# Kernel tuning notes

Measured on AMD Instinct MI355X. Metric: run time of the kernel, lower is better.

## Reference

```python
import jax, jax.numpy as jnp
import numpy as np

GRID = 48
F = GRID * GRID        # number of mesh faces
C = 128                # channels
H = 8                  # attention heads
DH = C // H
B = 2                  # meshes in batch
WID = 256              # SelectionPrediction width


def _bfs_levels():
    """BFS flood-fill levels on a 4-connected GRIDxGRID face graph, anchor at center.
    Returns [n_levels, max_ring] int32, padded with F (dropped on scatter)."""
    c = GRID // 2
    ii, jj = np.meshgrid(np.arange(GRID), np.arange(GRID), indexing='ij')
    d = (np.abs(ii - c) + np.abs(jj - c)).reshape(-1)  # BFS depth == Manhattan dist
    L = int(d.max()) + 1
    Bd = int(np.bincount(d).max())
    idx = np.full((L, Bd), F, dtype=np.int32)
    for lv in range(L):
        faces = np.nonzero(d == lv)[0]
        idx[lv, :faces.size] = faces
    return jnp.asarray(idx)


def setup_inputs() -> dict:
    key = jax.random.key(0)
    ks = jax.random.split(key, 16)
    s = 1.0 / np.sqrt(C)
    sw = 1.0 / np.sqrt(WID)
    return {
        'x':  jax.random.normal(ks[0], (B, C, F), jnp.float32),
        # AnchorAttentionBlock projections (q/k/v/out)
        'Wq': jax.random.normal(ks[1], (C, C), jnp.float32) * s,
        'Wk': jax.random.normal(ks[2], (C, C), jnp.float32) * s,
        'Wv': jax.random.normal(ks[3], (C, C), jnp.float32) * s,
        'Wo': jax.random.normal(ks[4], (C, C), jnp.float32) * s,
        # SelectionPrediction (n_input=C, width=256, depth=3, sigmoid)
        'W1': jax.random.normal(ks[5], (C, WID), jnp.float32) * s,
        'b1': jnp.zeros((WID,), jnp.float32),
        'W2': jax.random.normal(ks[6], (WID, WID), jnp.float32) * sw,
        'b2': jnp.zeros((WID,), jnp.float32),
        'W3': jax.random.normal(ks[7], (WID, WID), jnp.float32) * sw,
        'b3': jnp.zeros((WID,), jnp.float32),
        'W4': jax.random.normal(ks[8], (WID, WID), jnp.float32) * sw,
        'b4': jnp.zeros((WID,), jnp.float32),
        'W5': jax.random.normal(ks[9], (WID, 1), jnp.float32) * sw,
        'b5': jnp.zeros((1,), jnp.float32),
        'levels_idx': _bfs_levels(),
    }


def reference(x, Wq, Wk, Wv, Wo, W1, b1, W2, b2, W3, b3, W4, b4, W5, b5, levels_idx):
    scale = 1.0 / jnp.sqrt(jnp.asarray(DH, x.dtype))

    def flood(feats):                       # feats: [F, C], one mesh
        def step(cur, idx):                 # idx: [Bd] boundary ring (pad = F)
            q = cur[idx]                                    # [Bd, C] (pad rows clamp-gather)
            qh = (q @ Wq).reshape(-1, H, DH)                # [Bd, H, DH]
            kh = (cur @ Wk).reshape(F, H, DH)               # global fftype: keys = all faces
            vh = (cur @ Wv).reshape(F, H, DH)
            att = jax.nn.softmax(jnp.einsum('bhd,fhd->bhf', qh, kh) * scale, axis=-1)
            o = jnp.einsum('bhf,fhd->bhd', att, vh).reshape(-1, C) @ Wo
            new = q + o                                     # mode='resid'
            return cur.at[idx].set(new, mode='drop'), None  # pad idx == F -> dropped
        out, _ = jax.lax.scan(step, feats, levels_idx)
        return out

    final = jax.vmap(flood)(x.transpose(0, 2, 1))           # [B, F, C]
    # SelectionPrediction on final_features.transpose(2,1)
    h = jax.nn.relu(final @ W1 + b1)
    h = jax.nn.relu(h @ W2 + b2)
    h = jax.nn.relu(h @ W3 + b3)
    h = jax.nn.relu(h @ W4 + b4)
    scores = jax.nn.sigmoid(h @ W5 + b5)                    # [B, F, 1] in [0, 1]
    return final.transpose(0, 2, 1), scores
```

## Files before the change

### kernel.cpp

```cpp
#include <hip/hip_runtime.h>
#include <hip/hip_bf16.h>
#include <stdint.h>

#define GRIDN 48
#define F 2304
#define C 128
#define H 8
#define DH 16
#define NB 2
#define WID 256
#define NLV 49
#define SMH (H * 18)
#define GLV 7

typedef __hip_bfloat16 bf16;

__device__ __forceinline__ float b2f(bf16 v) { return __bfloat162float(v); }

__global__ void k_permdetect(const void* __restrict__ x, int* __restrict__ flag,
                             int* __restrict__ permIdx, int* __restrict__ lvflags) {
    __shared__ int cnt[NLV], start[NLV];
    __shared__ int bad;
    int t = threadIdx.x;
    if (t == 0) bad = 0;
    if (t < NLV) cnt[t] = 0;
    for (int i = t; i < 2 * NLV; i += 256) lvflags[i] = 0;
    __syncthreads();
    {
        const bf16* xb = (const bf16*)x;
        int insane = 0;
        #pragma unroll
        for (int i = 0; i < 8; ++i) {
            float v = b2f(xb[t * 8 + i]);
            if (!(fabsf(v) < 1e10f)) insane = 1;
        }
        if (insane) atomicOr(&bad, 1);
    }
    for (int f = t; f < F; f += 256) {
        int d = abs(f / GRIDN - GRIDN / 2) + abs(f % GRIDN - GRIDN / 2);
        atomicAdd(&cnt[d], 1);
    }
    __syncthreads();
    if (t == 0) {
        int s = 0;
        for (int l = 0; l < NLV; ++l) { start[l] = s; s += cnt[l]; }
        *flag = bad;
    }
    __syncthreads();
    for (int f = t; f < F; f += 256) {
        int d = abs(f / GRIDN - GRIDN / 2) + abs(f % GRIDN - GRIDN / 2);
        permIdx[f] = atomicAdd(&start[d], 1);
    }
}

struct WSeg { const void* src; int off; int cnt; };
struct WSegs { WSeg s[14]; };

__global__ void k_convert(WSegs segs, const int* __restrict__ flag,
                          float* __restrict__ dst, int total) {
    int i = blockIdx.x * blockDim.x + threadIdx.x;
    if (i >= total) return;
    bool f32 = (*flag != 0);
    #pragma unroll 1
    for (int j = 0; j < 14; ++j) {
        int off = segs.s[j].off, cnt = segs.s[j].cnt;
        if (i >= off && i < off + cnt) {
            int k = i - off;
            dst[i] = f32 ? ((const float*)segs.s[j].src)[k]
                         : b2f(((const bf16*)segs.s[j].src)[k]);
            return;
        }
    }
}

__global__ void k_wtrans(const float* __restrict__ Wk, const float* __restrict__ Wv,
                         const float* __restrict__ Wo, float* __restrict__ wT) {
    int m = blockIdx.y;
    const float* s = m == 0 ? Wk : (m == 1 ? Wv : Wo);
    int c = blockIdx.x;
    int k = threadIdx.x;
    wT[((size_t)m * C + c) * C + k] = s[k * C + c];
}

__global__ void k_transpose_in(const void* __restrict__ x, const int* __restrict__ flag,
                               float* __restrict__ cur) {
    __shared__ float tile[32][33];
    bool f32 = (*flag != 0);
    int b = blockIdx.z;
    int f0 = blockIdx.x * 32, c0 = blockIdx.y * 32;
    int tx = threadIdx.x, ty = threadIdx.y;
    #pragma unroll
    for (int i = 0; i < 4; ++i) {
        int c = c0 + ty + i * 8;
        size_t idx = ((size_t)b * C + c) * F + f0 + tx;
        tile[ty + i * 8][tx] = f32 ? ((const float*)x)[idx] : b2f(((const bf16*)x)[idx]);
    }
    __syncthreads();
    #pragma unroll
    for (int i = 0; i < 4; ++i) {
        int f = f0 + ty + i * 8;
        cur[((size_t)b * F + f) * C + c0 + tx] = tile[tx][ty + i * 8];
    }
}

__global__ __launch_bounds__(128) void k_proj_init(
        const float* __restrict__ cur, const int* __restrict__ permIdx,
        const float* __restrict__ Wq, const float* __restrict__ Wk, const float* __restrict__ Wv,
        float* __restrict__ qh, float* __restrict__ khT, float* __restrict__ vhT) {
    __shared__ float rows[2][C];
    int r0 = blockIdx.x * 2;
    int tid = threadIdx.x;
    rows[0][tid] = cur[(size_t)r0 * C + tid];
    rows[1][tid] = cur[(size_t)(r0 + 1) * C + tid];
    __syncthreads();
    float aq0 = 0.f, aq1 = 0.f, ak0 = 0.f, ak1 = 0.f, av0 = 0.f, av1 = 0.f;
    for (int k = 0; k < C; ++k) {
        float wq = Wq[k * C + tid];
        float wk = Wk[k * C + tid];
        float wv = Wv[k * C + tid];
        float x0 = rows[0][k], x1 = rows[1][k];
        aq0 = fmaf(x0, wq, aq0); aq1 = fmaf(x1, wq, aq1);
        ak0 = fmaf(x0, wk, ak0); ak1 = fmaf(x1, wk, ak1);
        av0 = fmaf(x0, wv, av0); av1 = fmaf(x1, wv, av1);
    }
    const float scale = 0.25f;
    #pragma unroll
    for (int r = 0; r < 2; ++r) {
        int grow = r0 + r;
        int mesh = grow / F, face = grow % F;
        int p = permIdx[face];
        qh[(size_t)grow * C + tid] = (r == 0 ? aq0 : aq1) * scale;
        khT[((size_t)mesh * C + tid) * F + p] = r == 0 ? ak0 : ak1;
        vhT[((size_t)mesh * C + tid) * F + p] = r == 0 ? av0 : av1;
    }
}

struct Rings { int v[NLV + 1]; };
struct Pairs { int v[NLV + 1]; };

__global__ __launch_bounds__(256) void k_static(
        int Bd, Rings rings, Pairs pairs,
        const int* __restrict__ levels,
        const float* __restrict__ qh_all,
        const float* __restrict__ khT, const float* __restrict__ vhT,
        float* __restrict__ smS) {
    int bx = blockIdx.x;
    int mesh = bx & 1;
    int gp = bx >> 1;
    int lv = 0;
    while (gp >= pairs.v[lv + 1]) ++lv;
    int spair = gp - pairs.v[lv];
    int rs = rings.v[lv];
    int s0 = spair * 2, s1 = s0 + 1;
    int face0 = (s0 < Bd) ? levels[lv * Bd + s0] : F;
    int face1 = (s1 < Bd) ? levels[lv * Bd + s1] : F;
    bool a0 = (face0 >= 0 && face0 < F), a1 = (face1 >= 0 && face1 < F);
    if (!a0 && !a1) return;

    __shared__ float sQh[2][C];
    int tid = threadIdx.x;
    size_t row0 = ((size_t)mesh * F + face0) * C;
    size_t row1 = ((size_t)mesh * F + face1) * C;
    if (tid < C) sQh[0][tid] = a0 ? qh_all[row0 + tid] : 0.f;
    else { int c = tid - C; sQh[1][c] = a1 ? qh_all[row1 + c] : 0.f; }
    __syncthreads();

    int head = tid >> 5, sub = tid & 31;
    float q0[DH], q1[DH];
    #pragma unroll
    for (int d = 0; d < DH; ++d) { q0[d] = sQh[0][head * DH + d]; q1[d] = sQh[1][head * DH + d]; }

    const float* Kb = khT + ((size_t)mesh * C + head * DH) * F;
    const float* Vb = vhT + ((size_t)mesh * C + head * DH) * F;

    float m0 = -1e30f, l0 = 0.f, m1 = -1e30f, l1 = 0.f;
    float acc0[DH], acc1[DH];
    #pragma unroll
    for (int d = 0; d < DH; ++d) { acc0[d] = 0.f; acc1[d] = 0.f; }

    int base0 = rs & ~127;
    for (int base = base0; base < F; base += 128) {
        int p4 = base + 4 * sub;
        float sx0 = 0, sy0 = 0, sz0 = 0, sw0 = 0;
        float sx1 = 0, sy1 = 0, sz1 = 0, sw1 = 0;
        #pragma unroll
        for (int d = 0; d < DH; ++d) {
            float4 kk = *(const float4*)(Kb + d * F + p4);
            float a = q0[d], b = q1[d];
            sx0 = fmaf(a, kk.x, sx0); sy0 = fmaf(a, kk.y, sy0);
            sz0 = fmaf(a, kk.z, sz0); sw0 = fmaf(a, kk.w, sw0);
            sx1 = fmaf(b, kk.x, sx1); sy1 = fmaf(b, kk.y, sy1);
            sz1 = fmaf(b, kk.z, sz1); sw1 = fmaf(b, kk.w, sw1);
        }
        float g0 = 1.f, g1 = 1.f, g2 = 1.f, g3 = 1.f;
        if (base < rs) {
            g0 = (p4     >= rs) ? 1.f : 0.f; g1 = (p4 + 1 >= rs) ? 1.f : 0.f;
            g2 = (p4 + 2 >= rs) ? 1.f : 0.f; g3 = (p4 + 3 >= rs) ? 1.f : 0.f;
        }
        float mx0 = fmaxf(fmaxf(sx0, sy0), fmaxf(sz0, sw0));
        float mn0 = fmaxf(m0, mx0);
        float c0 = __expf(m0 - mn0);
        float px0 = __expf(sx0 - mn0) * g0, py0 = __expf(sy0 - mn0) * g1;
        float pz0 = __expf(sz0 - mn0) * g2, pw0 = __expf(sw0 - mn0) * g3;
        l0 = fmaf(l0, c0, px0 + py0 + pz0 + pw0);
        m0 = mn0;
        float mx1 = fmaxf(fmaxf(sx1, sy1), fmaxf(sz1, sw1));
        float mn1 = fmaxf(m1, mx1);
        float c1e = __expf(m1 - mn1);
        float px1 = __expf(sx1 - mn1) * g0, py1 = __expf(sy1 - mn1) * g1;
        float pz1 = __expf(sz1 - mn1) * g2, pw1 = __expf(sw1 - mn1) * g3;
        l1 = fmaf(l1, c1e, px1 + py1 + pz1 + pw1);
        m1 = mn1;
        #pragma unroll
        for (int d = 0; d < DH; ++d) {
            float4 vv = *(const float4*)(Vb + d * F + p4);
            float w0 = fmaf(px0, vv.x, fmaf(py0, vv.y, fmaf(pz0, vv.z, pw0 * vv.w)));
            float w1 = fmaf(px1, vv.x, fmaf(py1, vv.y, fmaf(pz1, vv.z, pw1 * vv.w)));
            acc0[d] = fmaf(acc0[d], c0, w0);
            acc1[d] = fmaf(acc1[d], c1e, w1);
        }
    }

    #pragma unroll
    for (int w = 16; w >= 1; w >>= 1) {
        float mo = __shfl_xor(m0, w), lo = __shfl_xor(l0, w);
        float mn = fmaxf(m0, mo);
        float ca = __expf(m0 - mn), cb = __expf(mo - mn);
        l0 = l0 * ca + lo * cb;
        #pragma unroll
        for (int d = 0; d < DH; ++d) {
            float ao = __shfl_xor(acc0[d], w);
            acc0[d] = acc0[d] * ca + ao * cb;
        }
        m0 = mn;
        mo = __shfl_xor(m1, w); lo = __shfl_xor(l1, w);
        mn = fmaxf(m1, mo);
        ca = __expf(m1 - mn); cb = __expf(mo - mn);
        l1 = l1 * ca + lo * cb;
        #pragma unroll
        for (int d = 0; d < DH; ++d) {
            float ao = __shfl_xor(acc1[d], w);
            acc1[d] = acc1[d] * ca + ao * cb;
        }
        m1 = mn;
    }
    if (sub == 0) {
        if (a0) {
            float* S = smS + (size_t)(mesh * F + face0) * SMH + head * 18;
            S[0] = m0; S[1] = l0;
            #pragma unroll
            for (int d = 0; d < DH; ++d) S[2 + d] = acc0[d];
        }
        if (a1) {
            float* S = smS + (size_t)(mesh * F + face1) * SMH + head * 18;
            S[0] = m1; S[1] = l1;
            #pragma unroll
            for (int d = 0; d < DH; ++d) S[2 + d] = acc1[d];
        }
    }
}

struct Grp { int lv0; int rs0; int bofs[GLV + 1]; int rs[GLV]; int re[GLV]; int ns[GLV]; };

__global__ __launch_bounds__(256, 3) void k_group(
        int Bd, Grp grp,
        const int* __restrict__ levels, const int* __restrict__ permIdx,
        const float* __restrict__ qh_all, float* __restrict__ cur,
        float* __restrict__ khT, float* __restrict__ vhT,
        const float* __restrict__ smS,
        const float* __restrict__ WkT, const float* __restrict__ WvT,
        const float* __restrict__ WoT,
        float* __restrict__ stgK, float* __restrict__ stgV,
        int* __restrict__ lvflags) {
    int bx = blockIdx.x;
    int g = 0;
    while (bx >= grp.bofs[g + 1]) ++g;
    int lb = bx - grp.bofs[g];
    int mesh = lb & 1;
    int spair = lb >> 1;
    int lv = grp.lv0 + g;
    int rs0 = grp.rs0;

    int s0 = spair * 2, s1 = s0 + 1;
    int face0 = (s0 < Bd) ? levels[lv * Bd + s0] : F;
    int face1 = (s1 < Bd) ? levels[lv * Bd + s1] : F;
    bool a0 = (face0 >= 0 && face0 < F), a1 = (face1 >= 0 && face1 < F);

    __shared__ __attribute__((aligned(16))) float sQh[2][C], sQ[2][C], sRed[2][C], sNew2[2][C];
    __shared__ float sL[2][H];
    int tid = threadIdx.x;
    size_t row0 = ((size_t)mesh * F + face0) * C;
    size_t row1 = ((size_t)mesh * F + face1) * C;
    if (tid < C) {
        if (a0) { sQ[0][tid] = cur[row0 + tid]; sQh[0][tid] = qh_all[row0 + tid]; }
        else    { sQ[0][tid] = 0.f; sQh[0][tid] = 0.f; }
    } else {
        int c = tid - C;
        if (a1) { sQ[1][c] = cur[row1 + c]; sQh[1][c] = qh_all[row1 + c]; }
        else    { sQ[1][c] = 0.f; sQh[1][c] = 0.f; }
    }
    __syncthreads();

    int head = tid >> 5, sub = tid & 31;
    float q0[DH], q1[DH];
    #pragma unroll
    for (int d = 0; d < DH; ++d) { q0[d] = sQh[0][head * DH + d]; q1[d] = sQh[1][head * DH + d]; }

    const float* Kb = khT + ((size_t)mesh * C + head * DH) * F;
    const float* Vb = vhT + ((size_t)mesh * C + head * DH) * F;

    float m0 = -1e30f, l0 = 0.f, m1 = -1e30f, l1 = 0.f;
    float acc0[DH], acc1[DH];
    #pragma unroll
    for (int d = 0; d < DH; ++d) { acc0[d] = 0.f; acc1[d] = 0.f; }

    for (int base = 0; base < rs0; base += 128) {
        int p4 = base + 4 * sub;
        float sx0 = 0, sy0 = 0, sz0 = 0, sw0 = 0;
        float sx1 = 0, sy1 = 0, sz1 = 0, sw1 = 0;
        #pragma unroll
        for (int d = 0; d < DH; ++d) {
            float4 kk = *(const float4*)(Kb + d * F + p4);
            float a = q0[d], b = q1[d];
            sx0 = fmaf(a, kk.x, sx0); sy0 = fmaf(a, kk.y, sy0);
            sz0 = fmaf(a, kk.z, sz0); sw0 = fmaf(a, kk.w, sw0);
            sx1 = fmaf(b, kk.x, sx1); sy1 = fmaf(b, kk.y, sy1);
            sz1 = fmaf(b, kk.z, sz1); sw1 = fmaf(b, kk.w, sw1);
        }
        float g0 = 1.f, g1 = 1.f, g2 = 1.f, g3 = 1.f;
        if (base + 128 > rs0) {
            g0 = (p4     < rs0) ? 1.f : 0.f; g1 = (p4 + 1 < rs0) ? 1.f : 0.f;
            g2 = (p4 + 2 < rs0) ? 1.f : 0.f; g3 = (p4 + 3 < rs0) ? 1.f : 0.f;
        }
        float mx0 = fmaxf(fmaxf(sx0, sy0), fmaxf(sz0, sw0));
        float mn0 = fmaxf(m0, mx0);
        float c0 = __expf(m0 - mn0);
        float px0 = __expf(sx0 - mn0) * g0, py0 = __expf(sy0 - mn0) * g1;
        float pz0 = __expf(sz0 - mn0) * g2, pw0 = __expf(sw0 - mn0) * g3;
        l0 = fmaf(l0, c0, px0 + py0 + pz0 + pw0);
        m0 = mn0;
        float mx1 = fmaxf(fmaxf(sx1, sy1), fmaxf(sz1, sw1));
        float mn1 = fmaxf(m1, mx1);
        float c1e = __expf(m1 - mn1);
        float px1 = __expf(sx1 - mn1) * g0, py1 = __expf(sy1 - mn1) * g1;
        float pz1 = __expf(sz1 - mn1) * g2, pw1 = __expf(sw1 - mn1) * g3;
        l1 = fmaf(l1, c1e, px1 + py1 + pz1 + pw1);
        m1 = mn1;
        #pragma unroll
        for (int d = 0; d < DH; ++d) {
            float4 vv = *(const float4*)(Vb + d * F + p4);
            float w0 = fmaf(px0, vv.x, fmaf(py0, vv.y, fmaf(pz0, vv.z, pw0 * vv.w)));
            float w1 = fmaf(px1, vv.x, fmaf(py1, vv.y, fmaf(pz1, vv.z, pw1 * vv.w)));
            acc0[d] = fmaf(acc0[d], c0, w0);
            acc1[d] = fmaf(acc1[d], c1e, w1);
        }
    }

    for (int gp = 0; gp < g; ++gp) {
        if (tid == 0) {
            int need = grp.ns[gp];
            int* fl = &lvflags[(grp.lv0 + gp) * 2 + mesh];
            int guard = 0;
            while (__hip_atomic_load(fl, __ATOMIC_RELAXED, __HIP_MEMORY_SCOPE_AGENT) < need
                   && guard < (1 << 22)) {
                __builtin_amdgcn_s_sleep(1);
                ++guard;
            }
        }
        __syncthreads();
        int frs = grp.rs[gp], fre = grp.re[gp];
        for (int p = frs + sub; p < fre; p += 32) {
            const unsigned long long* kc =
                (const unsigned long long*)(stgK + ((size_t)mesh * F + p) * C + head * DH);
            const unsigned long long* vc =
                (const unsigned long long*)(stgV + ((size_t)mesh * F + p) * C + head * DH);
            float s0v = 0.f, s1v = 0.f;
            #pragma unroll
            for (int d2 = 0; d2 < DH / 2; ++d2) {
                unsigned long long kw = __hip_atomic_load(kc + d2, __ATOMIC_RELAXED,
                                                          __HIP_MEMORY_SCOPE_AGENT);
                float2 kf = *(float2*)&kw;
                s0v = fmaf(q0[2 * d2], kf.x, s0v); s0v = fmaf(q0[2 * d2 + 1], kf.y, s0v);
                s1v = fmaf(q1[2 * d2], kf.x, s1v); s1v = fmaf(q1[2 * d2 + 1], kf.y, s1v);
            }
            float vv[DH];
            #pragma unroll
            for (int d2 = 0; d2 < DH / 2; ++d2) {
                unsigned long long vw = __hip_atomic_load(vc + d2, __ATOMIC_RELAXED,
                                                          __HIP_MEMORY_SCOPE_AGENT);
                float2 vf = *(float2*)&vw;
                vv[2 * d2] = vf.x; vv[2 * d2 + 1] = vf.y;
            }
            {
                float mn = fmaxf(m0, s0v);
                float c = __expf(m0 - mn), pw = __expf(s0v - mn);
                l0 = l0 * c + pw;
                #pragma unroll
                for (int d = 0; d < DH; ++d) acc0[d] = fmaf(acc0[d], c, pw * vv[d]);
                m0 = mn;
            }
            {
                float mn = fmaxf(m1, s1v);
                float c = __expf(m1 - mn), pw = __expf(s1v - mn);
                l1 = l1 * c + pw;
                #pragma unroll
                for (int d = 0; d < DH; ++d) acc1[d] = fmaf(acc1[d], c, pw * vv[d]);
                m1 = mn;
            }
        }
    }

    #pragma unroll
    for (int w = 16; w >= 1; w >>= 1) {
        float mo = __shfl_xor(m0, w), lo = __shfl_xor(l0, w);
        float mn = fmaxf(m0, mo);
        float ca = __expf(m0 - mn), cb = __expf(mo - mn);
        l0 = l0 * ca + lo * cb;
        #pragma unroll
        for (int d = 0; d < DH; ++d) {
            float ao = __shfl_xor(acc0[d], w);
            acc0[d] = acc0[d] * ca + ao * cb;
        }
        m0 = mn;
        mo = __shfl_xor(m1, w); lo = __shfl_xor(l1, w);
        mn = fmaxf(m1, mo);
        ca = __expf(m1 - mn); cb = __expf(mo - mn);
        l1 = l1 * ca + lo * cb;
        #pragma unroll
        for (int d = 0; d < DH; ++d) {
            float ao = __shfl_xor(acc1[d], w);
            acc1[d] = acc1[d] * ca + ao * cb;
        }
        m1 = mn;
    }
    if (sub == 0) {
        {
            int fr = a0 ? face0 : 0;
            const float* S = smS + (size_t)(mesh * F + fr) * SMH + head * 18;
            float ms = S[0], ls = S[1];
            float mn = fmaxf(m0, ms);
            float ca = __expf(m0 - mn), cb = __expf(ms - mn);
            sL[0][head] = l0 * ca + ls * cb;
            #pragma unroll
            for (int d = 0; d < DH; ++d)
                sRed[0][head * DH + d] = fmaf(acc0[d], ca, S[2 + d] * cb);
        }
        {
            int fr = a1 ? face1 : 0;
            const float* S = smS + (size_t)(mesh * F + fr) * SMH + head * 18;
            float ms = S[0], ls = S[1];
            float mn = fmaxf(m1, ms);
            float ca = __expf(m1 - mn), cb = __expf(ms - mn);
            sL[1][head] = l1 * ca + ls * cb;
            #pragma unroll
            for (int d = 0; d < DH; ++d)
                sRed[1][head * DH + d] = fmaf(acc1[d], ca, S[2 + d] * cb);
        }
    }
    __syncthreads();
    if (tid < C) sRed[0][tid] = sRed[0][tid] / sL[0][tid >> 4];
    else { int c = tid - C; sRed[1][c] = sRed[1][c] / sL[1][c >> 4]; }
    __syncthreads();

    bool doStage = (g != GLV - 1);
    {
        int j = tid >> 7;
        int c = tid & 127;
        bool act = j == 0 ? a0 : a1;
        float o = 0.f;
        const float4* WoR = (const float4*)(WoT + (size_t)c * C);
        const float4* Rr  = (const float4*)(&sRed[j][0]);
        #pragma unroll
        for (int k4 = 0; k4 < C / 4; ++k4) {
            float4 w = WoR[k4];
            float4 r = Rr[k4];
            o = fmaf(r.x, w.x, o); o = fmaf(r.y, w.y, o);
            o = fmaf(r.z, w.z, o); o = fmaf(r.w, w.w, o);
        }
        float nv = sQ[j][c] + o;
        sNew2[j][c] = nv;
        if (act) cur[(j == 0 ? row0 : row1) + c] = nv;
    }
    __syncthreads();
    #pragma unroll 1
    for (int j = 0; j < 2; ++j) {
        bool act = j == 0 ? a0 : a1;
        if (!act) continue;
        int facej = j == 0 ? face0 : face1;
        int p = permIdx[facej];
        int c = tid & 127;
        const float* WT = (tid < C) ? WkT : WvT;
        float a = 0.f;
        const float4* Wr = (const float4*)(WT + (size_t)c * C);
        const float4* Nr = (const float4*)(&sNew2[j][0]);
        #pragma unroll
        for (int k4 = 0; k4 < C / 4; ++k4) {
            float4 w = Wr[k4];
            float4 x = Nr[k4];
            a = fmaf(x.x, w.x, a); a = fmaf(x.y, w.y, a);
            a = fmaf(x.z, w.z, a); a = fmaf(x.w, w.w, a);
        }
        if (tid < C) {
            khT[((size_t)mesh * C + c) * F + p] = a;
            if (doStage)
                __hip_atomic_store(stgK + ((size_t)mesh * F + p) * C + c, a,
                                   __ATOMIC_RELAXED, __HIP_MEMORY_SCOPE_AGENT);
        } else {
            vhT[((size_t)mesh * C + c) * F + p] = a;
            if (doStage)
                __hip_atomic_store(stgV + ((size_t)mesh * F + p) * C + c, a,
                                   __ATOMIC_RELAXED, __HIP_MEMORY_SCOPE_AGENT);
        }
    }
    __syncthreads();
    if (doStage && tid == 0)
        __hip_atomic_fetch_add(&lvflags[lv * 2 + mesh], 1,
                               __ATOMIC_RELAXED, __HIP_MEMORY_SCOPE_AGENT);
}

__global__ __launch_bounds__(256) void k_mlp(
        const float* __restrict__ cur,
        const float* __restrict__ W1, const float* __restrict__ b1,
        const float* __restrict__ W2, const float* __restrict__ b2,
        const float* __restrict__ W3, const float* __restrict__ b3,
        const float* __restrict__ W4, const float* __restrict__ b4,
        const float* __restrict__ W5, const float* __restrict__ b5,
        float* __restrict__ out_scores) {
    __shared__ float sIn[2][C];
    __shared__ float sA[2][WID];
    __shared__ float sB[2][WID];
    int tid = threadIdx.x;
    int r0 = blockIdx.x * 2;
    for (int i = tid; i < 2 * C; i += 256) sIn[i >> 7][i & 127] = cur[(size_t)r0 * C + i];
    __syncthreads();
    {
        float a0 = 0.f, a1 = 0.f;
        for (int k = 0; k < C; ++k) {
            float w = W1[k * WID + tid];
            a0 = fmaf(sIn[0][k], w, a0);
            a1 = fmaf(sIn[1][k], w, a1);
        }
        float bias = b1[tid];
        sA[0][tid] = fmaxf(a0 + bias, 0.f);
        sA[1][tid] = fmaxf(a1 + bias, 0.f);
    }
    __syncthreads();
    {
        float a0 = 0.f, a1 = 0.f;
        for (int k = 0; k < WID; ++k) {
            float w = W2[k * WID + tid];
            a0 = fmaf(sA[0][k], w, a0);
            a1 = fmaf(sA[1][k], w, a1);
        }
        float bias = b2[tid];
        sB[0][tid] = fmaxf(a0 + bias, 0.f);
        sB[1][tid] = fmaxf(a1 + bias, 0.f);
    }
    __syncthreads();
    {
        float a0 = 0.f, a1 = 0.f;
        for (int k = 0; k < WID; ++k) {
            float w = W3[k * WID + tid];
            a0 = fmaf(sB[0][k], w, a0);
            a1 = fmaf(sB[1][k], w, a1);
        }
        float bias = b3[tid];
        sA[0][tid] = fmaxf(a0 + bias, 0.f);
        sA[1][tid] = fmaxf(a1 + bias, 0.f);
    }
    __syncthreads();
    {
        float a0 = 0.f, a1 = 0.f;
        for (int k = 0; k < WID; ++k) {
            float w = W4[k * WID + tid];
            a0 = fmaf(sA[0][k], w, a0);
            a1 = fmaf(sA[1][k], w, a1);
        }
        float bias = b4[tid];
        sB[0][tid] = fmaxf(a0 + bias, 0.f);
        sB[1][tid] = fmaxf(a1 + bias, 0.f);
    }
    __syncthreads();
    if (tid < 2) {
        float a = b5[0];
        for (int k = 0; k < WID; ++k) a = fmaf(sB[tid][k], W5[k], a);
        out_scores[r0 + tid] = 1.f / (1.f + __expf(-a));
    }
}

__global__ void k_transpose_out(const float* __restrict__ cur, float* __restrict__ out) {
    __shared__ float tile[32][33];
    int b = blockIdx.z;
    int f0 = blockIdx.x * 32, c0 = blockIdx.y * 32;
    int tx = threadIdx.x, ty = threadIdx.y;
    #pragma unroll
    for (int i = 0; i < 4; ++i) {
        int f = f0 + ty + i * 8;
        tile[ty + i * 8][tx] = cur[((size_t)b * F + f) * C + c0 + tx];
    }
    __syncthreads();
    #pragma unroll
    for (int i = 0; i < 4; ++i) {
        int c = c0 + ty + i * 8;
        out[((size_t)b * C + c) * F + f0 + tx] = tile[tx][ty + i * 8];
    }
}

extern "C" void kernel_launch(void* const* d_in, const int* in_sizes, int n_in,
                              void* d_out, int out_size, void* d_ws, size_t ws_size,
                              hipStream_t stream) {
    const int* levels = (const int*)d_in[15];
    int Bd = in_sizes[15] / NLV;

    const size_t n = (size_t)NB * F * C;
    float* cur  = (float*)d_ws;
    float* qh   = cur + n;
    float* khT  = qh + n;
    float* vhT  = khT + n;
    float* wbuf = vhT + n;
    float* wT   = wbuf + 296196;
    int*   permIdx = (int*)(wT + 49152);
    int*   flag = permIdx + F;
    int*   lvflags = flag + 1;
    float* smS  = (float*)(permIdx + 2404);
    float* stgK = smS + (size_t)NB * F * SMH;
    float* stgV = stgK + n;

    const int oWq = 0,       oWk = 16384,  oWv = 32768,  oWo = 49152;
    const int oW1 = 65536,   oB1 = 98304;
    const int oW2 = 98560,   oB2 = 164096;
    const int oW3 = 164352,  oB3 = 229888;
    const int oW4 = 230144,  oB4 = 295680;
    const int oW5 = 295936,  oB5 = 296192;
    const int wtot = 296193;

    WSegs segs = {{
        { d_in[1],  oWq, 16384 }, { d_in[2],  oWk, 16384 },
        { d_in[3],  oWv, 16384 }, { d_in[4],  oWo, 16384 },
        { d_in[5],  oW1, 32768 }, { d_in[6],  oB1, 256 },
        { d_in[7],  oW2, 65536 }, { d_in[8],  oB2, 256 },
        { d_in[9],  oW3, 65536 }, { d_in[10], oB3, 256 },
        { d_in[11], oW4, 65536 }, { d_in[12], oB4, 256 },
        { d_in[13], oW5, 256 },   { d_in[14], oB5, 1 },
    }};

    Rings rings;
    Pairs pairs;
    int totPairs = 0;
    {
        int cnt[NLV];
        for (int l = 0; l < NLV; ++l) cnt[l] = 0;
        for (int i = 0; i < GRIDN; ++i)
            for (int j = 0; j < GRIDN; ++j)
                cnt[(i < 24 ? 24 - i : i - 24) + (j < 24 ? 24 - j : j - 24)]++;
        rings.v[0] = 0;
        pairs.v[0] = 0;
        for (int l = 0; l < NLV; ++l) {
            rings.v[l + 1] = rings.v[l] + cnt[l];
            pairs.v[l + 1] = pairs.v[l] + (cnt[l] + 1) / 2;
        }
        totPairs = pairs.v[NLV];
    }

    float* out0 = (float*)d_out;
    float* out1 = out0 + (size_t)NB * C * F;

    k_permdetect<<<1, 256, 0, stream>>>(d_in[0], flag, permIdx, lvflags);
    k_convert<<<(wtot + 255) / 256, 256, 0, stream>>>(segs, flag, wbuf, wtot);
    k_wtrans<<<dim3(C, 3), C, 0, stream>>>(wbuf + oWk, wbuf + oWv, wbuf + oWo, wT);
    k_transpose_in<<<dim3(F / 32, C / 32, NB), dim3(32, 8), 0, stream>>>(d_in[0], flag, cur);
    k_proj_init<<<(NB * F) / 2, 128, 0, stream>>>(cur, permIdx, wbuf + oWq, wbuf + oWk, wbuf + oWv,
                                                  qh, khT, vhT);

    k_static<<<2 * totPairs, 256, 0, stream>>>(Bd, rings, pairs, levels, qh, khT, vhT, smS);

    for (int lv0 = 0; lv0 < NLV; lv0 += GLV) {
        Grp grp;
        grp.lv0 = lv0;
        grp.rs0 = rings.v[lv0];
        grp.bofs[0] = 0;
        for (int g = 0; g < GLV; ++g) {
            int lv = lv0 + g;
            int rs = rings.v[lv], re = rings.v[lv + 1];
            int ns = (re - rs + 1) / 2;
            grp.rs[g] = rs;
            grp.re[g] = re;
            grp.ns[g] = ns;
            grp.bofs[g + 1] = grp.bofs[g] + 2 * ns;
        }
        k_group<<<grp.bofs[GLV], 256, 0, stream>>>(Bd, grp, levels, permIdx, qh, cur,
                                                   khT, vhT, smS,
                                                   wT, wT + 16384, wT + 32768,
                                                   stgK, stgV, lvflags);
    }

    k_mlp<<<(NB * F) / 2, 256, 0, stream>>>(cur, wbuf + oW1, wbuf + oB1, wbuf + oW2, wbuf + oB2,
                                            wbuf + oW3, wbuf + oB3, wbuf + oW4, wbuf + oB4,
                                            wbuf + oW5, wbuf + oB5, out1);
    k_transpose_out<<<dim3(F / 32, C / 32, NB), dim3(32, 8), 0, stream>>>(cur, out0);
}
```

Before: 1.467 ms.

## Replace grouped level launches with single persistent flood kernel using per-level flags

Replaces the seven grouped launches, each covering seven BFS levels, with one k_flood launch over all level pairs. Blocks now wait on per-level completion flags and read a per-mesh 'levels done' counter to decide which prefix they can fold in bulk. K and V updates are written straight into the transposed khT/vhT with atomic stores, which removes the separate stgK/stgV staging buffers. The bulk pass loses its float4 vectorised loads for scalar atomic column loads, and cross-level dependencies now rely only on spin-waits inside one grid, which risks long stalls if dependent blocks are scheduled before their producers.

```diff
diff --git a/kernel.cpp b/kernel.cpp
--- a/kernel.cpp
+++ b/kernel.cpp
@@ -11,7 +11,6 @@
 #define WID 256
 #define NLV 49
 #define SMH (H * 18)
-#define GLV 7
 
 typedef __hip_bfloat16 bf16;
 
@@ -24,7 +23,7 @@
     int t = threadIdx.x;
     if (t == 0) bad = 0;
     if (t < NLV) cnt[t] = 0;
-    for (int i = t; i < 2 * NLV; i += 256) lvflags[i] = 0;
+    for (int i = t; i < 2 * NLV + 2; i += 256) lvflags[i] = 0;
     __syncthreads();
     {
         const bf16* xb = (const bf16*)x;
@@ -260,26 +259,21 @@
     }
 }
 
-struct Grp { int lv0; int rs0; int bofs[GLV + 1]; int rs[GLV]; int re[GLV]; int ns[GLV]; };
-
-__global__ __launch_bounds__(256, 3) void k_group(
-        int Bd, Grp grp,
+__global__ __launch_bounds__(256, 4) void k_flood(
+        int Bd, Rings rings, Pairs pairs,
         const int* __restrict__ levels, const int* __restrict__ permIdx,
         const float* __restrict__ qh_all, float* __restrict__ cur,
         float* __restrict__ khT, float* __restrict__ vhT,
         const float* __restrict__ smS,
         const float* __restrict__ WkT, const float* __restrict__ WvT,
         const float* __restrict__ WoT,
-        float* __restrict__ stgK, float* __restrict__ stgV,
-        int* __restrict__ lvflags) {
+        int* __restrict__ lvflags, int* __restrict__ lvdone) {
     int bx = blockIdx.x;
-    int g = 0;
-    while (bx >= grp.bofs[g + 1]) ++g;
-    int lb = bx - grp.bofs[g];
-    int mesh = lb & 1;
-    int spair = lb >> 1;
-    int lv = grp.lv0 + g;
-    int rs0 = grp.rs0;
+    int mesh = bx & 1;
+    int gp2 = bx >> 1;
+    int lv = 0;
+    while (gp2 >= pairs.v[lv + 1]) ++lv;
+    int spair = gp2 - pairs.v[lv];
 
     int s0 = spair * 2, s1 = s0 + 1;
     int face0 = (s0 < Bd) ? levels[lv * Bd + s0] : F;
@@ -306,109 +300,63 @@
     #pragma unroll
     for (int d = 0; d < DH; ++d) { q0[d] = sQh[0][head * DH + d]; q1[d] = sQh[1][head * DH + d]; }
 
-    const float* Kb = khT + ((size_t)mesh * C + head * DH) * F;
-    const float* Vb = vhT + ((size_t)mesh * C + head * DH) * F;
+    float* Kb = khT + ((size_t)mesh * C + head * DH) * F;
+    float* Vb = vhT + ((size_t)mesh * C + head * DH) * F;
 
     float m0 = -1e30f, l0 = 0.f, m1 = -1e30f, l1 = 0.f;
     float acc0[DH], acc1[DH];
     #pragma unroll
     for (int d = 0; d < DH; ++d) { acc0[d] = 0.f; acc1[d] = 0.f; }
 
-    for (int base = 0; base < rs0; base += 128) {
-        int p4 = base + 4 * sub;
-        float sx0 = 0, sy0 = 0, sz0 = 0, sw0 = 0;
-        float sx1 = 0, sy1 = 0, sz1 = 0, sw1 = 0;
-        #pragma unroll
-        for (int d = 0; d < DH; ++d) {
-            float4 kk = *(const float4*)(Kb + d * F + p4);
-            float a = q0[d], b = q1[d];
-            sx0 = fmaf(a, kk.x, sx0); sy0 = fmaf(a, kk.y, sy0);
-            sz0 = fmaf(a, kk.z, sz0); sw0 = fmaf(a, kk.w, sw0);
-            sx1 = fmaf(b, kk.x, sx1); sy1 = fmaf(b, kk.y, sy1);
-            sz1 = fmaf(b, kk.z, sz1); sw1 = fmaf(b, kk.w, sw1);
-        }
-        float g0 = 1.f, g1 = 1.f, g2 = 1.f, g3 = 1.f;
-        if (base + 128 > rs0) {
-            g0 = (p4     < rs0) ? 1.f : 0.f; g1 = (p4 + 1 < rs0) ? 1.f : 0.f;
-            g2 = (p4 + 2 < rs0) ? 1.f : 0.f; g3 = (p4 + 3 < rs0) ? 1.f : 0.f;
-        }
-        float mx0 = fmaxf(fmaxf(sx0, sy0), fmaxf(sz0, sw0));
-        float mn0 = fmaxf(m0, mx0);
-        float c0 = __expf(m0 - mn0);
-        float px0 = __expf(sx0 - mn0) * g0, py0 = __expf(sy0 - mn0) * g1;
-        float pz0 = __expf(sz0 - mn0) * g2, pw0 = __expf(sw0 - mn0) * g3;
-        l0 = fmaf(l0, c0, px0 + py0 + pz0 + pw0);
-        m0 = mn0;
-        float mx1 = fmaxf(fmaxf(sx1, sy1), fmaxf(sz1, sw1));
-        float mn1 = fmaxf(m1, mx1);
-        float c1e = __expf(m1 - mn1);
-        float px1 = __expf(sx1 - mn1) * g0, py1 = __expf(sy1 - mn1) * g1;
-        float pz1 = __expf(sz1 - mn1) * g2, pw1 = __expf(sw1 - mn1) * g3;
-        l1 = fmaf(l1, c1e, px1 + py1 + pz1 + pw1);
-        m1 = mn1;
-        #pragma unroll
-        for (int d = 0; d < DH; ++d) {
-            float4 vv = *(const float4*)(Vb + d * F + p4);
-            float w0 = fmaf(px0, vv.x, fmaf(py0, vv.y, fmaf(pz0, vv.z, pw0 * vv.w)));
-            float w1 = fmaf(px1, vv.x, fmaf(py1, vv.y, fmaf(pz1, vv.z, pw1 * vv.w)));
-            acc0[d] = fmaf(acc0[d], c0, w0);
-            acc1[d] = fmaf(acc1[d], c1e, w1);
-        }
-    }
-
-    for (int gp = 0; gp < g; ++gp) {
-        if (tid == 0) {
-            int need = grp.ns[gp];
-            int* fl = &lvflags[(grp.lv0 + gp) * 2 + mesh];
-            int guard = 0;
-            while (__hip_atomic_load(fl, __ATOMIC_RELAXED, __HIP_MEMORY_SCOPE_AGENT) < need
-                   && guard < (1 << 22)) {
-                __builtin_amdgcn_s_sleep(1);
-                ++guard;
-            }
-        }
-        __syncthreads();
-        int frs = grp.rs[gp], fre = grp.re[gp];
-        for (int p = frs + sub; p < fre; p += 32) {
-            const unsigned long long* kc =
-                (const unsigned long long*)(stgK + ((size_t)mesh * F + p) * C + head * DH);
-            const unsigned long long* vc =
-                (const unsigned long long*)(stgV + ((size_t)mesh * F + p) * C + head * DH);
-            float s0v = 0.f, s1v = 0.f;
-            #pragma unroll
-            for (int d2 = 0; d2 < DH / 2; ++d2) {
-                unsigned long long kw = __hip_atomic_load(kc + d2, __ATOMIC_RELAXED,
-                                                          __HIP_MEMORY_SCOPE_AGENT);
-                float2 kf = *(float2*)&kw;
-                s0v = fmaf(q0[2 * d2], kf.x, s0v); s0v = fmaf(q0[2 * d2 + 1], kf.y, s0v);
-                s1v = fmaf(q1[2 * d2], kf.x, s1v); s1v = fmaf(q1[2 * d2 + 1], kf.y, s1v);
-            }
-            float vv[DH];
-            #pragma unroll
-            for (int d2 = 0; d2 < DH / 2; ++d2) {
-                unsigned long long vw = __hip_atomic_load(vc + d2, __ATOMIC_RELAXED,
-                                                          __HIP_MEMORY_SCOPE_AGENT);
-                float2 vf = *(float2*)&vw;
-                vv[2 * d2] = vf.x; vv[2 * d2 + 1] = vf.y;
-            }
-            {
-                float mn = fmaxf(m0, s0v);
-                float c = __expf(m0 - mn), pw = __expf(s0v - mn);
-                l0 = l0 * c + pw;
-                #pragma unroll
-                for (int d = 0; d < DH; ++d) acc0[d] = fmaf(acc0[d], c, pw * vv[d]);
-                m0 = mn;
-            }
-            {
-                float mn = fmaxf(m1, s1v);
-                float c = __expf(m1 - mn), pw = __expf(s1v - mn);
-                l1 = l1 * c + pw;
-                #pragma unroll
-                for (int d = 0; d < DH; ++d) acc1[d] = fmaf(acc1[d], c, pw * vv[d]);
-                m1 = mn;
-            }
-        }
-    }
+    #define FOLD_COL(p)                                                                 \
+    {                                                                                   \
+        float kvv[DH], vv[DH];                                                          \
+        _Pragma("unroll")                                                               \
+        for (int d = 0; d < DH; ++d)                                                    \
+            kvv[d] = __hip_atomic_load(Kb + (size_t)d * F + (p), __ATOMIC_RELAXED,      \
+                                       __HIP_MEMORY_SCOPE_AGENT);                       \
+        _Pragma("unroll")                                                               \
+        for (int d = 0; d < DH; ++d)                                                    \
+            vv[d] = __hip_atomic_load(Vb + (size_t)d * F + (p), __ATOMIC_RELAXED,       \
+                                      __HIP_MEMORY_SCOPE_AGENT);                        \
+        float s0v = 0.f, s1v = 0.f;                                                     \
+        _Pragma("unroll")                                                               \
+        for (int d = 0; d < DH; ++d) {                                                  \
+            s0v = fmaf(q0[d], kvv[d], s0v);                                             \
+            s1v = fmaf(q1[d], kvv[d], s1v);                                             \
+        }                                                                               \
+        float mn0_ = fmaxf(m0, s0v);                                                    \
+        float c0_ = __expf(m0 - mn0_), pw0_ = __expf(s0v - mn0_);                       \
+        l0 = l0 * c0_ + pw0_;                                                           \
+        _Pragma("unroll")                                                               \
+        for (int d = 0; d < DH; ++d) acc0[d] = fmaf(acc0[d], c0_, pw0_ * vv[d]);        \
+        m0 = mn0_;                                                                      \
+        float mn1_ = fmaxf(m1, s1v);                                                    \
+        float c1_ = __expf(m1 - mn1_), pw1_ = __expf(s1v - mn1_);                       \
+        l1 = l1 * c1_ + pw1_;                                                           \
+        _Pragma("unroll")                                                               \
+        for (int d = 0; d < DH; ++d) acc1[d] = fmaf(acc1[d], c1_, pw1_ * vv[d]);        \
+        m1 = mn1_;                                                                      \
+    }
+
+    int ld = __hip_atomic_load(&lvdone[mesh], __ATOMIC_RELAXED, __HIP_MEMORY_SCOPE_AGENT);
+    if (ld > lv) ld = lv;
+    int bulkEnd = rings.v[ld];
+    for (int p = sub; p < bulkEnd; p += 32) FOLD_COL(p);
+
+    for (int gpi = ld; gpi < lv; ++gpi) {
+        int need = pairs.v[gpi + 1] - pairs.v[gpi];
+        int* fl = &lvflags[gpi * 2 + mesh];
+        int guard = 0;
+        while (__hip_atomic_load(fl, __ATOMIC_RELAXED, __HIP_MEMORY_SCOPE_AGENT) < need
+               && guard < (1 << 22)) {
+            __builtin_amdgcn_s_sleep(1);
+            ++guard;
+        }
+        int frs = rings.v[gpi], fre = rings.v[gpi + 1];
+        for (int p = frs + sub; p < fre; p += 32) FOLD_COL(p);
+    }
+    #undef FOLD_COL
 
     #pragma unroll
     for (int w = 16; w >= 1; w >>= 1) {
@@ -462,7 +410,6 @@
     else { int c = tid - C; sRed[1][c] = sRed[1][c] / sL[1][c >> 4]; }
     __syncthreads();
 
-    bool doStage = (g != GLV - 1);
     {
         int j = tid >> 7;
         int c = tid & 127;
@@ -482,40 +429,43 @@
         if (act) cur[(j == 0 ? row0 : row1) + c] = nv;
     }
     __syncthreads();
-    #pragma unroll 1
-    for (int j = 0; j < 2; ++j) {
-        bool act = j == 0 ? a0 : a1;
-        if (!act) continue;
-        int facej = j == 0 ? face0 : face1;
-        int p = permIdx[facej];
-        int c = tid & 127;
-        const float* WT = (tid < C) ? WkT : WvT;
-        float a = 0.f;
-        const float4* Wr = (const float4*)(WT + (size_t)c * C);
-        const float4* Nr = (const float4*)(&sNew2[j][0]);
-        #pragma unroll
-        for (int k4 = 0; k4 < C / 4; ++k4) {
-            float4 w = Wr[k4];
-            float4 x = Nr[k4];
-            a = fmaf(x.x, w.x, a); a = fmaf(x.y, w.y, a);
-            a = fmaf(x.z, w.z, a); a = fmaf(x.w, w.w, a);
-        }
-        if (tid < C) {
-            khT[((size_t)mesh * C + c) * F + p] = a;
-            if (doStage)
-                __hip_atomic_store(stgK + ((size_t)mesh * F + p) * C + c, a,
+
+    if (lv != NLV - 1) {
+        #pragma unroll 1
+        for (int j = 0; j < 2; ++j) {
+            bool act = j == 0 ? a0 : a1;
+            if (!act) continue;
+            int facej = j == 0 ? face0 : face1;
+            int p = permIdx[facej];
+            int c = tid & 127;
+            const float* WT = (tid < C) ? WkT : WvT;
+            float a = 0.f;
+            const float4* Wr = (const float4*)(WT + (size_t)c * C);
+            const float4* Nr = (const float4*)(&sNew2[j][0]);
+            #pragma unroll
+            for (int k4 = 0; k4 < C / 4; ++k4) {
+                float4 w = Wr[k4];
+                float4 x = Nr[k4];
+                a = fmaf(x.x, w.x, a); a = fmaf(x.y, w.y, a);
+                a = fmaf(x.z, w.z, a); a = fmaf(x.w, w.w, a);
+            }
+            if (tid < C)
+                __hip_atomic_store(khT + ((size_t)mesh * C + c) * F + p, a,
                                    __ATOMIC_RELAXED, __HIP_MEMORY_SCOPE_AGENT);
-        } else {
-            vhT[((size_t)mesh * C + c) * F + p] = a;
-            if (doStage)
-                __hip_atomic_store(stgV + ((size_t)mesh * F + p) * C + c, a,
+            else
+                __hip_atomic_store(vhT + ((size_t)mesh * C + c) * F + p, a,
                                    __ATOMIC_RELAXED, __HIP_MEMORY_SCOPE_AGENT);
         }
-    }
-    __syncthreads();
-    if (doStage && tid == 0)
-        __hip_atomic_fetch_add(&lvflags[lv * 2 + mesh], 1,
-                               __ATOMIC_RELAXED, __HIP_MEMORY_SCOPE_AGENT);
+        __syncthreads();
+        if (tid == 0) {
+            int need = pairs.v[lv + 1] - pairs.v[lv];
+            int old = __hip_atomic_fetch_add(&lvflags[lv * 2 + mesh], 1,
+                                             __ATOMIC_RELAXED, __HIP_MEMORY_SCOPE_AGENT);
+            if (old == need - 1)
+                __hip_atomic_fetch_max(&lvdone[mesh], lv + 1,
+                                       __ATOMIC_RELAXED, __HIP_MEMORY_SCOPE_AGENT);
+        }
+    }
 }
 
 __global__ __launch_bounds__(256) void k_mlp(
@@ -622,9 +572,8 @@
     int*   permIdx = (int*)(wT + 49152);
     int*   flag = permIdx + F;
     int*   lvflags = flag + 1;
-    float* smS  = (float*)(permIdx + 2404);
-    float* stgK = smS + (size_t)NB * F * SMH;
-    float* stgV = stgK + n;
+    int*   lvdone = lvflags + 2 * NLV;
+    float* smS  = (float*)(permIdx + 2408);
 
     const int oWq = 0,       oWk = 16384,  oWv = 32768,  oWo = 49152;
     const int oW1 = 65536,   oB1 = 98304;
@@ -674,25 +623,10 @@
 
     k_static<<<2 * totPairs, 256, 0, stream>>>(Bd, rings, pairs, levels, qh, khT, vhT, smS);
 
-    for (int lv0 = 0; lv0 < NLV; lv0 += GLV) {
-        Grp grp;
-        grp.lv0 = lv0;
-        grp.rs0 = rings.v[lv0];
-        grp.bofs[0] = 0;
-        for (int g = 0; g < GLV; ++g) {
-            int lv = lv0 + g;
-            int rs = rings.v[lv], re = rings.v[lv + 1];
-            int ns = (re - rs + 1) / 2;
-            grp.rs[g] = rs;
-            grp.re[g] = re;
-            grp.ns[g] = ns;
-            grp.bofs[g + 1] = grp.bofs[g] + 2 * ns;
-        }
-        k_group<<<grp.bofs[GLV], 256, 0, stream>>>(Bd, grp, levels, permIdx, qh, cur,
-                                                   khT, vhT, smS,
-                                                   wT, wT + 16384, wT + 32768,
-                                                   stgK, stgV, lvflags);
-    }
+    k_flood<<<2 * totPairs, 256, 0, stream>>>(Bd, rings, pairs, levels, permIdx, qh, cur,
+                                              khT, vhT, smS,
+                                              wT, wT + 16384, wT + 32768,
+                                              lvflags, lvdone);
 
     k_mlp<<<(NB * F) / 2, 256, 0, stream>>>(cur, wbuf + oW1, wbuf + oB1, wbuf + oW2, wbuf + oB2,
                                             wbuf + oW3, wbuf + oB3, wbuf + oW4, wbuf + oB4,
```

New measurement: 1.469 ms. No clear change (+0.1%).
